# Kernel tuning notes

Hardware: AMD Instinct MI355X
Metric: run time of the kernel (lower is better)

Reference implementation:

```python
import jax, jax.numpy as jnp
import numpy as np

MUL0, MUL1, MUL2, NMOD = 128, 64, 32, 2  # multiplicities of 0e,1e,2e and modalities
D0, D1, D2 = MUL0, MUL1 * 3, MUL2 * 5     # 128, 192, 160 -> total 480


def setup_inputs() -> dict:
    key = jax.random.key(0)
    ks = jax.random.split(key, 7)
    N, G = 200000, 512
    x = jax.random.normal(ks[0], (N, D0 + D1 + D2), dtype=jnp.float32)
    modal_attr = jax.random.uniform(ks[1], (G, NMOD), dtype=jnp.float32)
    W0 = jax.random.normal(ks[2], (MUL0, MUL0), dtype=jnp.float32)
    W0m = jax.random.normal(ks[3], (NMOD, MUL0), dtype=jnp.float32)
    W1 = jax.random.normal(ks[4], (MUL1, MUL1), dtype=jnp.float32)
    W2 = jax.random.normal(ks[5], (MUL2, MUL2), dtype=jnp.float32)
    batch = jnp.sort(jax.random.randint(ks[6], (N,), 0, G, dtype=jnp.int64))
    return {"x": x, "modal_attr": modal_attr, "W0": W0, "W0m": W0m,
            "W1": W1, "W2": W2, "batch": batch}


def reference(x, modal_attr, W0, W0m, W1, W2, batch):
    N = x.shape[0]
    # modality one-hot gathered per node and concatenated (appended 2x0e irrep)
    modal = modal_attr[batch]  # [N, NMOD]
    x0 = x[:, :D0]                                   # [N, 128]  0e
    x1 = x[:, D0:D0 + D1].reshape(N, MUL1, 3)        # [N, 64, 3] 1e
    x2 = x[:, D0 + D1:].reshape(N, MUL2, 5)          # [N, 32, 5] 2e
    # e3nn Linear: per-(l,p) block linear, paths summed, /sqrt(total fan-in mul)
    inv0 = 1.0 / np.sqrt(MUL0 + NMOD).astype(np.float32)
    out0 = (x0 @ W0 + modal @ W0m) * inv0            # [N, 128]
    out1 = jnp.einsum('nim,io->nom', x1, W1) * (1.0 / np.sqrt(MUL1).astype(np.float32))
    out2 = jnp.einsum('nim,io->nom', x2, W2) * (1.0 / np.sqrt(MUL2).astype(np.float32))
    return jnp.concatenate([out0, out1.reshape(N, D1), out2.reshape(N, D2)], axis=1)
```

## Files before the change

### kernel.cpp

```cpp
#include <hip/hip_runtime.h>
#include <hip/hip_bf16.h>


typedef __attribute__((ext_vector_type(8))) short  short8;
typedef __attribute__((ext_vector_type(4))) float  f32x4;

#define NTH 256
#define BR  32

#define W0H 0
#define W0L 16384
#define W1H 32768
#define W1L 36864
#define W2H 40960
#define W2L 41984

__device__ __forceinline__ unsigned bc2(__hip_bfloat162 h) {
    unsigned u; __builtin_memcpy(&u, &h, 4); return u;
}

struct HL4 { uint2 h, l; };

__device__ __forceinline__ HL4 split4(float a, float b, float c, float d) {
    __hip_bfloat162 h01 = __float22bfloat162_rn({a, b});
    __hip_bfloat162 h23 = __float22bfloat162_rn({c, d});
    float ra = a - __low2float(h01),  rb = b - __high2float(h01);
    float rc = c - __low2float(h23),  rd = d - __high2float(h23);
    __hip_bfloat162 l01 = __float22bfloat162_rn({ra, rb});
    __hip_bfloat162 l23 = __float22bfloat162_rn({rc, rd});
    HL4 r;
    r.h = make_uint2(bc2(h01), bc2(h23));
    r.l = make_uint2(bc2(l01), bc2(l23));
    return r;
}

__device__ __forceinline__ void packhl(const HL4& p, const HL4& q,
                                       short8& hi, short8& lo) {
    uint4 h4 = make_uint4(p.h.x, p.h.y, q.h.x, q.h.y);
    uint4 l4 = make_uint4(p.l.x, p.l.y, q.l.x, q.l.y);
    __builtin_memcpy(&hi, &h4, 16);
    __builtin_memcpy(&lo, &l4, 16);
}

__device__ __forceinline__ void split_w(float v, unsigned short& h, unsigned short& l) {
    __hip_bfloat16 hb = __float2bfloat16(v);
    float r = v - __bfloat162float(hb);
    __hip_bfloat16 lb = __float2bfloat16(r);
    __builtin_memcpy(&h, &hb, 2);
    __builtin_memcpy(&l, &lb, 2);
}

__device__ __forceinline__ void dma16(const float* g, char* lds_base) {
    __builtin_amdgcn_global_load_lds(
        (const __attribute__((address_space(1))) unsigned int*)g,
        (__attribute__((address_space(3))) unsigned int*)lds_base,
        16, 0, 0);
}

__global__ void prep_weights(const float* __restrict__ W0,
                             const float* __restrict__ W1,
                             const float* __restrict__ W2,
                             unsigned short* __restrict__ ws) {
    const int s0     = blockIdx.x * blockDim.x + threadIdx.x;
    const int STRIDE = gridDim.x * blockDim.x;
    for (int s = s0; s < 16384; s += STRIDE) {
        int j = s & 7, l = (s >> 3) & 63, kt = (s >> 9) & 3, ct = s >> 11;
        int col = ct * 16 + (l & 15);
        int k   = kt * 32 + (l >> 4) * 8 + j;
        unsigned short h, lo;
        split_w(W0[k * 128 + col], h, lo);
        ws[W0H + s] = h; ws[W0L + s] = lo;
    }
    for (int s = s0; s < 4096; s += STRIDE) {
        int j = s & 7, l = (s >> 3) & 63, kt = (s >> 9) & 1, ct = s >> 10;
        int col = ct * 16 + (l & 15);
        int k   = kt * 32 + (l >> 4) * 8 + j;
        unsigned short h, lo;
        split_w(W1[k * 64 + col], h, lo);
        ws[W1H + s] = h; ws[W1L + s] = lo;
    }
    for (int s = s0; s < 1024; s += STRIDE) {
        int j = s & 7, l = (s >> 3) & 63, ct = s >> 9;
        int col = ct * 16 + (l & 15);
        int k   = (l >> 4) * 8 + j;
        unsigned short h, lo;
        split_w(W2[k * 32 + col], h, lo);
        ws[W2H + s] = h; ws[W2L + s] = lo;
    }
}

#define MFMA(a, b, c) __builtin_amdgcn_mfma_f32_16x16x32_bf16((a), (b), (c), 0, 0, 0)

__global__ __launch_bounds__(NTH, 3) void irreps_mfma_kernel(
    const float* __restrict__ x,
    const float* __restrict__ modal_attr,
    const float* __restrict__ W0m,
    const unsigned short* __restrict__ wsf,
    const int*   __restrict__ batch,
    float*       __restrict__ out,
    int N)
{
    __shared__ __align__(16) char ldsb[49664];
    char*  raw  = ldsb;
    float* ldsf = reinterpret_cast<float*>(ldsb + 24576);

    const int tid  = threadIdx.x;
    const int w    = tid >> 6;
    const int l    = tid & 63;
    const int r    = l & 15;
    const int kg   = l >> 4;
    const int rb0  = (w >> 1) * 16;
    const int ch   = w & 1;
    const int row0 = blockIdx.x * BR;
    const int arow = rb0 + r;
    const int sw   = (arow & 7) << 4;

    #pragma unroll
    for (int i = 0; i < 4; ++i) {
        int c   = w * 4 + i;
        int o   = c * 1024 + l * 16;
        int row = o >> 9;
        int so  = o ^ ((row & 7) << 4);
        int col = so & 511;
        int n   = row0 + row; n = n < N ? n : N - 1;
        dma16(x + (size_t)n * 480 + (col >> 2), raw + c * 1024);
    }

    float am0[4], am1[4];
    #pragma unroll
    for (int reg = 0; reg < 4; ++reg) {
        int n  = row0 + rb0 + kg * 4 + reg;
        int nc = n < N ? n : N - 1;
        int g  = batch[nc];
        am0[reg] = modal_attr[2 * g];
        am1[reg] = modal_attr[2 * g + 1];
    }
    __syncthreads();

    short8 xah[4], xal[4];
    #pragma unroll
    for (int kt = 0; kt < 4; ++kt) {
        int b0 = arow * 512 + kt * 128 + kg * 32;
        f32x4 a = *reinterpret_cast<const f32x4*>(raw + (b0 ^ sw));
        f32x4 b = *reinterpret_cast<const f32x4*>(raw + ((b0 + 16) ^ sw));
        HL4 p = split4(a[0], a[1], a[2], a[3]);
        HL4 q = split4(b[0], b[1], b[2], b[3]);
        packhl(p, q, xah[kt], xal[kt]);
    }
    __syncthreads();

    #pragma unroll
    for (int i = 0; i < 6; ++i) {
        int c   = w * 6 + i;
        int o   = c * 1024 + l * 16;
        int row = o / 768;
        int so  = o ^ ((row & 7) << 4);
        int col = so - row * 768;
        int n   = row0 + row; n = n < N ? n : N - 1;
        dma16(x + (size_t)n * 480 + 128 + (col >> 2), raw + c * 1024);
    }
    {
        #pragma unroll
        for (int ci = 0; ci < 4; ++ci) {
            int ct = ch * 4 + ci;
            f32x4 acc = {0.f, 0.f, 0.f, 0.f};
            #pragma unroll
            for (int kt = 0; kt < 4; ++kt) {
                int b = ct * 4 + kt;
                short8 bh = *reinterpret_cast<const short8*>(wsf + W0H + (size_t)(b * 64 + l) * 8);
                short8 bl = *reinterpret_cast<const short8*>(wsf + W0L + (size_t)(b * 64 + l) * 8);
                acc = MFMA(xah[kt], bh, acc);
                acc = MFMA(xal[kt], bh, acc);
                acc = MFMA(xah[kt], bl, acc);
            }
            int col = ct * 16 + r;
            float wm0 = W0m[col], wm1 = W0m[128 + col];
            #pragma unroll
            for (int reg = 0; reg < 4; ++reg)
                ldsf[(rb0 + kg * 4 + reg) * 132 + col] =
                    (acc[reg] + am0[reg] * wm0 + am1[reg] * wm1) * 0.08770580193070293f;
        }
    }
    __syncthreads();

    short8 xbh[3][2], xbl[3][2];
    #pragma unroll
    for (int kt = 0; kt < 2; ++kt) {
        int b0 = arow * 768 + kt * 384 + kg * 96;
        float f[24];
        #pragma unroll
        for (int q = 0; q < 6; ++q) {
            f32x4 v = *reinterpret_cast<const f32x4*>(raw + ((b0 + q * 16) ^ sw));
            f[q * 4 + 0] = v[0]; f[q * 4 + 1] = v[1];
            f[q * 4 + 2] = v[2]; f[q * 4 + 3] = v[3];
        }
        #pragma unroll
        for (int m = 0; m < 3; ++m) {
            HL4 p = split4(f[0 + m], f[3 + m], f[6 + m],  f[9 + m]);
            HL4 q = split4(f[12 + m], f[15 + m], f[18 + m], f[21 + m]);
            packhl(p, q, xbh[m][kt], xbl[m][kt]);
        }
    }
    {
        #pragma unroll
        for (int j = 0; j < 4; ++j) {
            int idx = tid + j * NTH;
            int row = idx >> 5, c4 = idx & 31;
            int n   = row0 + row;
            if (n < N)
                *reinterpret_cast<float4*>(out + (size_t)n * 480 + c4 * 4) =
                    *reinterpret_cast<const float4*>(ldsf + row * 132 + c4 * 4);
        }
    }
    __syncthreads();

    #pragma unroll
    for (int i = 0; i < 5; ++i) {
        int c   = w * 5 + i;
        int o   = c * 1024 + l * 16;
        int row = o / 640;
        int so  = o ^ ((row & 7) << 4);
        int col = so - row * 640;
        int n   = row0 + row; n = n < N ? n : N - 1;
        dma16(x + (size_t)n * 480 + 320 + (col >> 2), raw + c * 1024);
    }
    {
        #pragma unroll
        for (int ci = 0; ci < 2; ++ci) {
            int ct = ch * 2 + ci;
            short8 bh[2], bl[2];
            #pragma unroll
            for (int kt = 0; kt < 2; ++kt) {
                int b = ct * 2 + kt;
                bh[kt] = *reinterpret_cast<const short8*>(wsf + W1H + (size_t)(b * 64 + l) * 8);
                bl[kt] = *reinterpret_cast<const short8*>(wsf + W1L + (size_t)(b * 64 + l) * 8);
            }
            #pragma unroll
            for (int m = 0; m < 3; ++m) {
                f32x4 acc = {0.f, 0.f, 0.f, 0.f};
                #pragma unroll
                for (int kt = 0; kt < 2; ++kt) {
                    acc = MFMA(xbh[m][kt], bh[kt], acc);
                    acc = MFMA(xbl[m][kt], bh[kt], acc);
                    acc = MFMA(xbh[m][kt], bl[kt], acc);
                }
                int col = 3 * (ct * 16 + r) + m;
                #pragma unroll
                for (int reg = 0; reg < 4; ++reg)
                    ldsf[(rb0 + kg * 4 + reg) * 196 + col] = acc[reg] * 0.125f;
            }
        }
    }
    __syncthreads();

    short8 xch[5], xcl[5];
    {
        int b0 = arow * 640 + kg * 160;
        float f[40];
        #pragma unroll
        for (int q = 0; q < 10; ++q) {
            f32x4 v = *reinterpret_cast<const f32x4*>(raw + ((b0 + q * 16) ^ sw));
            f[q * 4 + 0] = v[0]; f[q * 4 + 1] = v[1];
            f[q * 4 + 2] = v[2]; f[q * 4 + 3] = v[3];
        }
        #pragma unroll
        for (int m = 0; m < 5; ++m) {
            HL4 p = split4(f[0 + m],  f[5 + m],  f[10 + m], f[15 + m]);
            HL4 q = split4(f[20 + m], f[25 + m], f[30 + m], f[35 + m]);
            packhl(p, q, xch[m], xcl[m]);
        }
    }
    {
        #pragma unroll
        for (int j = 0; j < 6; ++j) {
            int idx = tid + j * NTH;
            int row = idx / 48, c4 = idx - row * 48;
            int n   = row0 + row;
            if (n < N)
                *reinterpret_cast<float4*>(out + (size_t)n * 480 + 128 + c4 * 4) =
                    *reinterpret_cast<const float4*>(ldsf + row * 196 + c4 * 4);
        }
    }
    __syncthreads();

    {
        int ct = ch;
        short8 bh = *reinterpret_cast<const short8*>(wsf + W2H + (size_t)(ct * 64 + l) * 8);
        short8 bl = *reinterpret_cast<const short8*>(wsf + W2L + (size_t)(ct * 64 + l) * 8);
        #pragma unroll
        for (int m = 0; m < 5; ++m) {
            f32x4 acc = {0.f, 0.f, 0.f, 0.f};
            acc = MFMA(xch[m], bh, acc);
            acc = MFMA(xcl[m], bh, acc);
            acc = MFMA(xch[m], bl, acc);
            int col = 5 * (ct * 16 + r) + m;
            #pragma unroll
            for (int reg = 0; reg < 4; ++reg)
                ldsf[(rb0 + kg * 4 + reg) * 164 + col] = acc[reg] * 0.17677669529663687f;
        }
    }
    __syncthreads();

    {
        #pragma unroll
        for (int j = 0; j < 5; ++j) {
            int idx = tid + j * NTH;
            int row = idx / 40, c4 = idx - row * 40;
            int n   = row0 + row;
            if (n < N)
                *reinterpret_cast<float4*>(out + (size_t)n * 480 + 320 + c4 * 4) =
                    *reinterpret_cast<const float4*>(ldsf + row * 164 + c4 * 4);
        }
    }
}

extern "C" void kernel_launch(void* const* d_in, const int* in_sizes, int n_in,
                              void* d_out, int out_size, void* d_ws, size_t ws_size,
                              hipStream_t stream) {
    const float* x     = (const float*)d_in[0];
    const float* modal = (const float*)d_in[1];
    const float* W0    = (const float*)d_in[2];
    const float* W0m   = (const float*)d_in[3];
    const float* W1    = (const float*)d_in[4];
    const float* W2    = (const float*)d_in[5];
    const int*   batch = (const int*)d_in[6];
    float* out = (float*)d_out;
    unsigned short* ws = (unsigned short*)d_ws;

    const int N    = in_sizes[6];
    const int grid = (N + BR - 1) / BR;

    prep_weights<<<84, NTH, 0, stream>>>(W0, W1, W2, ws);
    irreps_mfma_kernel<<<grid, NTH, 0, stream>>>(x, modal, W0m, ws, batch, out, N);
}
```

Measured before the change: 174.7 us.

## Load x directly into registers and double-buffer output staging in LDS

Replaces the staged global_load_lds DMA of each x segment into swizzled LDS with direct per-thread float4 global loads into registers, issued early for the 0e and 1e blocks and mid-kernel for the 2e block. The output staging now alternates between two LDS regions, which removes several block barriers and lets output stores overlap with the next block's MFMA work. This trades LDS traffic and syncs for much higher register pressure (30 float4 held live). That pressure may cut occupancy under the 3-block launch bound, and the per-lane global loads are less coalesced.

```diff
diff --git a/kernel.cpp b/kernel.cpp
--- a/kernel.cpp
+++ b/kernel.cpp
@@ -48,13 +48,6 @@
     __hip_bfloat16 lb = __float2bfloat16(r);
     __builtin_memcpy(&h, &hb, 2);
     __builtin_memcpy(&l, &lb, 2);
-}
-
-__device__ __forceinline__ void dma16(const float* g, char* lds_base) {
-    __builtin_amdgcn_global_load_lds(
-        (const __attribute__((address_space(1))) unsigned int*)g,
-        (__attribute__((address_space(3))) unsigned int*)lds_base,
-        16, 0, 0);
 }
 
 __global__ void prep_weights(const float* __restrict__ W0,
@@ -100,9 +93,9 @@
     float*       __restrict__ out,
     int N)
 {
-    __shared__ __align__(16) char ldsb[49664];
-    char*  raw  = ldsb;
-    float* ldsf = reinterpret_cast<float*>(ldsb + 24576);
+    __shared__ __align__(16) char ldsb[46080];
+    float* ldsA = reinterpret_cast<float*>(ldsb);
+    float* ldsB = reinterpret_cast<float*>(ldsb + 20992);
 
     const int tid  = threadIdx.x;
     const int w    = tid >> 6;
@@ -113,17 +106,24 @@
     const int ch   = w & 1;
     const int row0 = blockIdx.x * BR;
     const int arow = rb0 + r;
-    const int sw   = (arow & 7) << 4;
-
-    #pragma unroll
-    for (int i = 0; i < 4; ++i) {
-        int c   = w * 4 + i;
-        int o   = c * 1024 + l * 16;
-        int row = o >> 9;
-        int so  = o ^ ((row & 7) << 4);
-        int col = so & 511;
-        int n   = row0 + row; n = n < N ? n : N - 1;
-        dma16(x + (size_t)n * 480 + (col >> 2), raw + c * 1024);
+
+    const int nrow = (row0 + arow) < N ? (row0 + arow) : (N - 1);
+    const float* __restrict__ xr = x + (size_t)nrow * 480;
+
+    float4 araw[8];
+    #pragma unroll
+    for (int kt = 0; kt < 4; ++kt) {
+        const float* p = xr + kt * 32 + kg * 8;
+        araw[2 * kt]     = *reinterpret_cast<const float4*>(p);
+        araw[2 * kt + 1] = *reinterpret_cast<const float4*>(p + 4);
+    }
+    float4 braw[12];
+    #pragma unroll
+    for (int kt = 0; kt < 2; ++kt) {
+        const float* p = xr + 128 + (kt * 32 + kg * 8) * 3;
+        #pragma unroll
+        for (int q = 0; q < 6; ++q)
+            braw[kt * 6 + q] = *reinterpret_cast<const float4*>(p + q * 4);
     }
 
     float am0[4], am1[4];
@@ -135,30 +135,16 @@
         am0[reg] = modal_attr[2 * g];
         am1[reg] = modal_attr[2 * g + 1];
     }
-    __syncthreads();
 
     short8 xah[4], xal[4];
     #pragma unroll
     for (int kt = 0; kt < 4; ++kt) {
-        int b0 = arow * 512 + kt * 128 + kg * 32;
-        f32x4 a = *reinterpret_cast<const f32x4*>(raw + (b0 ^ sw));
-        f32x4 b = *reinterpret_cast<const f32x4*>(raw + ((b0 + 16) ^ sw));
-        HL4 p = split4(a[0], a[1], a[2], a[3]);
-        HL4 q = split4(b[0], b[1], b[2], b[3]);
+        float4 a = araw[2 * kt], b = araw[2 * kt + 1];
+        HL4 p = split4(a.x, a.y, a.z, a.w);
+        HL4 q = split4(b.x, b.y, b.z, b.w);
         packhl(p, q, xah[kt], xal[kt]);
     }
-    __syncthreads();
-
-    #pragma unroll
-    for (int i = 0; i < 6; ++i) {
-        int c   = w * 6 + i;
-        int o   = c * 1024 + l * 16;
-        int row = o / 768;
-        int so  = o ^ ((row & 7) << 4);
-        int col = so - row * 768;
-        int n   = row0 + row; n = n < N ? n : N - 1;
-        dma16(x + (size_t)n * 480 + 128 + (col >> 2), raw + c * 1024);
-    }
+
     {
         #pragma unroll
         for (int ci = 0; ci < 4; ++ci) {
@@ -177,7 +163,7 @@
             float wm0 = W0m[col], wm1 = W0m[128 + col];
             #pragma unroll
             for (int reg = 0; reg < 4; ++reg)
-                ldsf[(rb0 + kg * 4 + reg) * 132 + col] =
+                ldsA[(rb0 + kg * 4 + reg) * 132 + col] =
                     (acc[reg] + am0[reg] * wm0 + am1[reg] * wm1) * 0.08770580193070293f;
         }
     }
@@ -186,45 +172,28 @@
     short8 xbh[3][2], xbl[3][2];
     #pragma unroll
     for (int kt = 0; kt < 2; ++kt) {
-        int b0 = arow * 768 + kt * 384 + kg * 96;
         float f[24];
         #pragma unroll
         for (int q = 0; q < 6; ++q) {
-            f32x4 v = *reinterpret_cast<const f32x4*>(raw + ((b0 + q * 16) ^ sw));
-            f[q * 4 + 0] = v[0]; f[q * 4 + 1] = v[1];
-            f[q * 4 + 2] = v[2]; f[q * 4 + 3] = v[3];
+            float4 v = braw[kt * 6 + q];
+            f[q * 4 + 0] = v.x; f[q * 4 + 1] = v.y; f[q * 4 + 2] = v.z; f[q * 4 + 3] = v.w;
         }
         #pragma unroll
         for (int m = 0; m < 3; ++m) {
-            HL4 p = split4(f[0 + m], f[3 + m], f[6 + m],  f[9 + m]);
+            HL4 p = split4(f[0 + m],  f[3 + m],  f[6 + m],  f[9 + m]);
             HL4 q = split4(f[12 + m], f[15 + m], f[18 + m], f[21 + m]);
             packhl(p, q, xbh[m][kt], xbl[m][kt]);
         }
     }
-    {
-        #pragma unroll
-        for (int j = 0; j < 4; ++j) {
-            int idx = tid + j * NTH;
-            int row = idx >> 5, c4 = idx & 31;
-            int n   = row0 + row;
-            if (n < N)
-                *reinterpret_cast<float4*>(out + (size_t)n * 480 + c4 * 4) =
-                    *reinterpret_cast<const float4*>(ldsf + row * 132 + c4 * 4);
-        }
-    }
-    __syncthreads();
-
-    #pragma unroll
-    for (int i = 0; i < 5; ++i) {
-        int c   = w * 5 + i;
-        int o   = c * 1024 + l * 16;
-        int row = o / 640;
-        int so  = o ^ ((row & 7) << 4);
-        int col = so - row * 640;
-        int n   = row0 + row; n = n < N ? n : N - 1;
-        dma16(x + (size_t)n * 480 + 320 + (col >> 2), raw + c * 1024);
-    }
-    {
+    float4 craw[10];
+    {
+        const float* p = xr + 320 + kg * 40;
+        #pragma unroll
+        for (int q = 0; q < 10; ++q)
+            craw[q] = *reinterpret_cast<const float4*>(p + q * 4);
+    }
+    {
+        const float inv1 = 0.125f;
         #pragma unroll
         for (int ci = 0; ci < 2; ++ci) {
             int ct = ch * 2 + ci;
@@ -247,27 +216,52 @@
                 int col = 3 * (ct * 16 + r) + m;
                 #pragma unroll
                 for (int reg = 0; reg < 4; ++reg)
-                    ldsf[(rb0 + kg * 4 + reg) * 196 + col] = acc[reg] * 0.125f;
+                    ldsB[(rb0 + kg * 4 + reg) * 196 + col] = acc[reg] * inv1;
             }
         }
     }
+    {
+        #pragma unroll
+        for (int j = 0; j < 4; ++j) {
+            int idx = tid + j * NTH;
+            int row = idx >> 5, c4 = idx & 31;
+            int n   = row0 + row;
+            if (n < N)
+                *reinterpret_cast<float4*>(out + (size_t)n * 480 + c4 * 4) =
+                    *reinterpret_cast<const float4*>(ldsA + row * 132 + c4 * 4);
+        }
+    }
     __syncthreads();
 
     short8 xch[5], xcl[5];
     {
-        int b0 = arow * 640 + kg * 160;
         float f[40];
         #pragma unroll
         for (int q = 0; q < 10; ++q) {
-            f32x4 v = *reinterpret_cast<const f32x4*>(raw + ((b0 + q * 16) ^ sw));
-            f[q * 4 + 0] = v[0]; f[q * 4 + 1] = v[1];
-            f[q * 4 + 2] = v[2]; f[q * 4 + 3] = v[3];
+            float4 v = craw[q];
+            f[q * 4 + 0] = v.x; f[q * 4 + 1] = v.y; f[q * 4 + 2] = v.z; f[q * 4 + 3] = v.w;
         }
         #pragma unroll
         for (int m = 0; m < 5; ++m) {
             HL4 p = split4(f[0 + m],  f[5 + m],  f[10 + m], f[15 + m]);
             HL4 q = split4(f[20 + m], f[25 + m], f[30 + m], f[35 + m]);
             packhl(p, q, xch[m], xcl[m]);
+        }
+    }
+    {
+        int ct = ch;
+        short8 bh = *reinterpret_cast<const short8*>(wsf + W2H + (size_t)(ct * 64 + l) * 8);
+        short8 bl = *reinterpret_cast<const short8*>(wsf + W2L + (size_t)(ct * 64 + l) * 8);
+        #pragma unroll
+        for (int m = 0; m < 5; ++m) {
+            f32x4 acc = {0.f, 0.f, 0.f, 0.f};
+            acc = MFMA(xch[m], bh, acc);
+            acc = MFMA(xcl[m], bh, acc);
+            acc = MFMA(xch[m], bl, acc);
+            int col = 5 * (ct * 16 + r) + m;
+            #pragma unroll
+            for (int reg = 0; reg < 4; ++reg)
+                ldsA[(rb0 + kg * 4 + reg) * 164 + col] = acc[reg] * 0.17677669529663687f;
         }
     }
     {
@@ -278,25 +272,7 @@
             int n   = row0 + row;
             if (n < N)
                 *reinterpret_cast<float4*>(out + (size_t)n * 480 + 128 + c4 * 4) =
-                    *reinterpret_cast<const float4*>(ldsf + row * 196 + c4 * 4);
-        }
-    }
-    __syncthreads();
-
-    {
-        int ct = ch;
-        short8 bh = *reinterpret_cast<const short8*>(wsf + W2H + (size_t)(ct * 64 + l) * 8);
-        short8 bl = *reinterpret_cast<const short8*>(wsf + W2L + (size_t)(ct * 64 + l) * 8);
-        #pragma unroll
-        for (int m = 0; m < 5; ++m) {
-            f32x4 acc = {0.f, 0.f, 0.f, 0.f};
-            acc = MFMA(xch[m], bh, acc);
-            acc = MFMA(xcl[m], bh, acc);
-            acc = MFMA(xch[m], bl, acc);
-            int col = 5 * (ct * 16 + r) + m;
-            #pragma unroll
-            for (int reg = 0; reg < 4; ++reg)
-                ldsf[(rb0 + kg * 4 + reg) * 164 + col] = acc[reg] * 0.17677669529663687f;
+                    *reinterpret_cast<const float4*>(ldsB + row * 196 + c4 * 4);
         }
     }
     __syncthreads();
@@ -309,7 +285,7 @@
             int n   = row0 + row;
             if (n < N)
                 *reinterpret_cast<float4*>(out + (size_t)n * 480 + 320 + c4 * 4) =
-                    *reinterpret_cast<const float4*>(ldsf + row * 164 + c4 * 4);
+                    *reinterpret_cast<const float4*>(ldsA + row * 164 + c4 * 4);
         }
     }
 }
```

New measurement: 223.1 us. 27.7% more time.
